# Optimization experiments

Measured on AMD Instinct MI355X. Metric: run time of the kernel, lower is better.

Reference implementation:

```python
import jax, jax.numpy as jnp
import numpy as np

N_QUBITS = 10
DEPTH = 3
KSIZE = 16
DILATION = 1
NFREQ = 8

I4 = np.eye(4, dtype=np.complex64)
XX4 = np.fliplr(np.eye(4)).astype(np.complex64)
YY4 = np.array([[0, 0, 0, -1], [0, 0, 1, 0], [0, 1, 0, 0], [-1, 0, 0, 0]], dtype=np.complex64)


def _u3(t, p, l):
    ct = jnp.cos(t / 2).astype(jnp.complex64)
    st = jnp.sin(t / 2).astype(jnp.complex64)
    ep, el = jnp.exp(1j * p), jnp.exp(1j * l)
    return jnp.stack([jnp.stack([ct, -el * st]), jnp.stack([ep * st, ep * el * ct])])


def _ising_zz(t):
    em, ep = jnp.exp(-0.5j * t), jnp.exp(0.5j * t)
    return jnp.diag(jnp.stack([em, ep, ep, em]))


def _ising_xx(t):
    return jnp.cos(t / 2) * I4 - 1j * jnp.sin(t / 2) * XX4


def _ising_yy(t):
    return jnp.cos(t / 2) * I4 - 1j * jnp.sin(t / 2) * YY4


def _cu3(t, p, l):
    # controlled-U3 (control = 1): deferred-measurement form of qml.cond(measure, U3)
    return jnp.eye(4, dtype=jnp.complex64).at[2:, 2:].set(_u3(t, p, l))


def _apply_1q(state, U, wire):
    s = jnp.moveaxis(state, 1 + wire, -1)
    if U.ndim == 3:  # per-sample gate (batched angles)
        s = jnp.einsum('bij,b...j->b...i', U, s)
    else:
        s = jnp.einsum('ij,...j->...i', U, s)
    return jnp.moveaxis(s, -1, 1 + wire)


def _apply_2q(state, U, w1, w2):
    s = jnp.moveaxis(state, (1 + w1, 1 + w2), (-2, -1))
    shp = s.shape
    s = s.reshape(shp[:-2] + (4,))
    s = jnp.einsum('ij,...j->...i', U, s)
    return jnp.moveaxis(s.reshape(shp), (-2, -1), (1 + w1, 1 + w2))


def _run_circuit(angles, freq_scale, conv_params, pool_params):
    Bm = angles.shape[0]
    state = jnp.zeros((Bm, 2 ** N_QUBITS), jnp.complex64).at[:, 0].set(1.0)
    state = state.reshape((Bm,) + (2,) * N_QUBITS)
    # frequency-matched encoding: RY(a) then RX(freq_scale * a), per-sample angles
    for i in range(N_QUBITS):
        a = angles[:, i]
        c = jnp.cos(a / 2).astype(jnp.complex64)
        s = jnp.sin(a / 2).astype(jnp.complex64)
        ry = jnp.stack([jnp.stack([c, -s], -1), jnp.stack([s, c], -1)], -2)
        state = _apply_1q(state, ry, i)
        b = freq_scale[i] * a
        cb = jnp.cos(b / 2).astype(jnp.complex64)
        sb = jnp.sin(b / 2).astype(jnp.complex64)
        rx = jnp.stack([jnp.stack([cb, -1j * sb], -1), jnp.stack([-1j * sb, cb], -1)], -2)
        state = _apply_1q(state, rx, i)
    wires = list(range(N_QUBITS))
    for layer in range(DEPTH):
        wp = conv_params[layer]
        nw = len(wires)
        for parity in (0, 1):
            for i2, w in enumerate(wires):
                if i2 % 2 == parity and i2 < nw - 1:
                    nxt = wires[i2 + 1]
                    state = _apply_1q(state, _u3(wp[i2, 0], wp[i2, 1], wp[i2, 2]), w)
                    state = _apply_1q(state, _u3(wp[i2 + 1, 3], wp[i2 + 1, 4], wp[i2 + 1, 5]), nxt)
                    state = _apply_2q(state, _ising_zz(wp[i2, 6]), w, nxt)
                    state = _apply_2q(state, _ising_yy(wp[i2, 7]), w, nxt)
                    state = _apply_2q(state, _ising_xx(wp[i2, 8]), w, nxt)
                    state = _apply_1q(state, _u3(wp[i2, 9], wp[i2, 10], wp[i2, 11]), w)
                    state = _apply_1q(state, _u3(wp[i2 + 1, 12], wp[i2 + 1, 13], wp[i2 + 1, 14]), nxt)
        pp = pool_params[layer]
        for i2, w in enumerate(wires):
            if i2 % 2 == 1:
                state = _apply_2q(state, _cu3(pp[i2 // 2, 0], pp[i2 // 2, 1], pp[i2 // 2, 2]), w, wires[i2 - 1])
        wires = wires[::2]
    p = jnp.abs(state) ** 2
    p = p.reshape(Bm, 2, -1).sum(-1)
    return p[:, 0] - p[:, 1]  # <Z_0>


def _forward(x, proj_w, proj_b, freq_scale, conv_params, pool_params, agg_weights):
    B, C, T = x.shape
    eff = DILATION * (KSIZE - 1)
    W = T - eff
    idx = jnp.arange(W)[:, None] + DILATION * jnp.arange(KSIZE)[None, :]  # [W,K]
    win = x[:, :, idx]  # [B,C,W,K]
    f = jnp.fft.rfft(win, axis=-1)[..., :NFREQ]  # [B,C,W,NF]
    feats = jnp.stack([jnp.log1p(jnp.abs(f)), jnp.angle(f) / jnp.pi], -1)  # [B,C,W,NF,2]
    feats = jnp.transpose(feats, (0, 2, 1, 3, 4)).reshape(B, W, -1)  # [B,W,C*NF*2]
    proj = jnp.tanh(feats @ proj_w.T + proj_b) * jnp.pi  # [B,W,n_qubits]
    ev = _run_circuit(proj.reshape(B * W, N_QUBITS), freq_scale, conv_params, pool_params)
    outs = ev.reshape(B, W)
    wts = jax.nn.softmax(agg_weights[:W])
    return (outs * wts[None, :]).sum(1)


def setup_inputs():
    key = jax.random.key(0)
    k = jax.random.split(key, 6)
    fft_dim = 22 * NFREQ * 2
    return {
        'x': jax.random.normal(k[0], (16, 22, 128), jnp.float32),
        'proj_w': jax.random.normal(k[1], (N_QUBITS, fft_dim), jnp.float32) / np.sqrt(fft_dim).astype(np.float32),
        'proj_b': jnp.zeros((N_QUBITS,), jnp.float32),
        'freq_scale': jnp.linspace(0.5, 3.0, N_QUBITS, dtype=jnp.float32),
        'conv_params': 0.1 * jax.random.normal(k[2], (DEPTH, N_QUBITS, 15), jnp.float32),
        'pool_params': 0.1 * jax.random.normal(k[3], (DEPTH, N_QUBITS // 2, 3), jnp.float32),
        'agg_weights': jnp.zeros((113,), jnp.float32),
    }


def reference(x, proj_w, proj_b, freq_scale, conv_params, pool_params, agg_weights):
    return _forward(x, proj_w, proj_b, freq_scale, conv_params, pool_params, agg_weights)
```

## Files before the change

### kernel.cpp

```cpp
#include <hip/hip_runtime.h>
#include <math.h>

#define NQ 10
#define WW 113
#define BB 16
#define CC 22
#define NF 8
#define FDIM 352
#define NS (BB*WW)
#define NGATE 23
#define SLOT(j) ((j) ^ (((j) >> 5) & 31))

#define WAVE_FENCE() do { \
    asm volatile("s_waitcnt lgkmcnt(0)" ::: "memory"); \
    __builtin_amdgcn_sched_barrier(0); \
} while (0)

__device__ __forceinline__ float2 cmul(float2 a, float2 b) {
    return make_float2(a.x*b.x - a.y*b.y, a.x*b.y + a.y*b.x);
}

__constant__ int G_KIND[NGATE]  = {0,0,0,0,0, 0,0,0,0, 1,1,1,1,1, 0,0,0,0, 1,1, 0,0, 1};
__constant__ int G_LAYER[NGATE] = {0,0,0,0,0, 0,0,0,0, 0,0,0,0,0, 1,1,1,1, 1,1, 2,2, 2};
__constant__ int G_IA[NGATE]    = {0,2,4,6,8, 1,3,5,7, 0,1,2,3,4, 0,2,1,3, 0,1, 0,1, 0};

__device__ void u3mat(float2* U, float th, float ph, float lm) {
    float ct, st, cp, sp, cl, sl;
    sincosf(th * 0.5f, &st, &ct);
    sincosf(ph, &sp, &cp);
    sincosf(lm, &sl, &cl);
    U[0] = make_float2(ct, 0.f);
    U[1] = make_float2(-cl * st, -sl * st);
    U[2] = make_float2(cp * st, sp * st);
    U[3] = make_float2((cp * cl - sp * sl) * ct, (sp * cl + cp * sl) * ct);
}

__device__ void mm4(float2* C, const float2* A, const float2* B) {
#pragma unroll
    for (int i = 0; i < 4; ++i)
#pragma unroll
        for (int j = 0; j < 4; ++j) {
            float2 acc = make_float2(0.f, 0.f);
#pragma unroll
            for (int k = 0; k < 4; ++k) {
                float2 p = cmul(A[i*4+k], B[k*4+j]);
                acc.x += p.x; acc.y += p.y;
            }
            C[i*4+j] = acc;
        }
}

__global__ __launch_bounds__(64) void prep_kernel(
    const float* __restrict__ conv,
    const float* __restrict__ pool,
    const float* __restrict__ aggw,
    float2* __restrict__ mats,
    float* __restrict__ wts,
    float* __restrict__ out)
{
    const int t = threadIdx.x;

    float a0 = (t < WW) ? aggw[t] : -1e30f;
    float a1 = (t + 64 < WW) ? aggw[t + 64] : -1e30f;
    float mx = fmaxf(a0, a1);
    for (int off = 32; off > 0; off >>= 1) mx = fmaxf(mx, __shfl_xor(mx, off));
    float e0 = (t < WW) ? expf(a0 - mx) : 0.f;
    float e1 = (t + 64 < WW) ? expf(a1 - mx) : 0.f;
    float es = e0 + e1;
    for (int off = 32; off > 0; off >>= 1) es += __shfl_xor(es, off);
    float inv = 1.0f / es;
    if (t < WW) wts[t] = e0 * inv;
    if (t + 64 < WW) wts[t + 64] = e1 * inv;
    if (t < BB) out[t] = 0.f;

    if (t >= NGATE) return;
    int kind = G_KIND[t], layer = G_LAYER[t], ia = G_IA[t];
    float2 F[16];
    if (kind == 0) {
        const float* wp = conv + layer * 150;
        float2 Uw0[4], Un0[4], Uw1[4], Un1[4];
        u3mat(Uw0, wp[ia*15+0], wp[ia*15+1], wp[ia*15+2]);
        u3mat(Un0, wp[(ia+1)*15+3], wp[(ia+1)*15+4], wp[(ia+1)*15+5]);
        u3mat(Uw1, wp[ia*15+9], wp[ia*15+10], wp[ia*15+11]);
        u3mat(Un1, wp[(ia+1)*15+12], wp[(ia+1)*15+13], wp[(ia+1)*15+14]);
        float2 Kpre[16], Kpost[16];
#pragma unroll
        for (int a = 0; a < 2; ++a)
#pragma unroll
        for (int b = 0; b < 2; ++b)
#pragma unroll
        for (int c = 0; c < 2; ++c)
#pragma unroll
        for (int d = 0; d < 2; ++d) {
            Kpre [(2*a+b)*4 + (2*c+d)] = cmul(Uw0[a*2+c], Un0[b*2+d]);
            Kpost[(2*a+b)*4 + (2*c+d)] = cmul(Uw1[a*2+c], Un1[b*2+d]);
        }
        float cz, sz, cy, sy, cx, sx;
        sincosf(wp[ia*15+6] * 0.5f, &sz, &cz);
        sincosf(wp[ia*15+7] * 0.5f, &sy, &cy);
        sincosf(wp[ia*15+8] * 0.5f, &sx, &cx);
        float2 Z[16], Y[16], X[16];
#pragma unroll
        for (int k = 0; k < 16; ++k) { Z[k] = make_float2(0,0); Y[k] = make_float2(0,0); X[k] = make_float2(0,0); }
        Z[0]  = make_float2(cz, -sz); Z[5]  = make_float2(cz, sz);
        Z[10] = make_float2(cz,  sz); Z[15] = make_float2(cz, -sz);
        Y[0] = Y[5] = Y[10] = Y[15] = make_float2(cy, 0);
        Y[0*4+3] = make_float2(0,  sy); Y[1*4+2] = make_float2(0, -sy);
        Y[2*4+1] = make_float2(0, -sy); Y[3*4+0] = make_float2(0,  sy);
        X[0] = X[5] = X[10] = X[15] = make_float2(cx, 0);
        X[0*4+3] = X[1*4+2] = X[2*4+1] = X[3*4+0] = make_float2(0, -sx);
        float2 T1[16], M[16], T2[16];
        mm4(T1, Y, Z);
        mm4(M, X, T1);
        mm4(T2, M, Kpre);
        mm4(F, Kpost, T2);
    } else {
        const float* pp = pool + layer * 15 + ia * 3;
        float2 U[4];
        u3mat(U, pp[0], pp[1], pp[2]);
#pragma unroll
        for (int k = 0; k < 16; ++k) F[k] = make_float2(0,0);
        F[0*4+0] = make_float2(1,0); F[1*4+1] = make_float2(1,0);
        F[2*4+2] = U[0]; F[2*4+3] = U[1];
        F[3*4+2] = U[2]; F[3*4+3] = U[3];
    }
#pragma unroll
    for (int k = 0; k < 16; ++k) mats[t*16 + k] = F[k];
}

template<int B3,int B2,int B1,int B0>
__device__ __forceinline__ int lanepart(int L) {
    constexpr int rm = (1<<B3)|(1<<B2)|(1<<B1)|(1<<B0);
    int idx = 0, lb = 5;
#pragma unroll
    for (int p = 9; p >= 0; --p)
        if (!((rm >> p) & 1)) { idx |= ((L >> lb) & 1) << p; --lb; }
    return idx;
}

template<int B3,int B2,int B1,int B0>
__device__ __forceinline__ int rpart(int r) {
    return (((r>>3)&1)<<B3) | (((r>>2)&1)<<B2) | (((r>>1)&1)<<B1) | ((r&1)<<B0);
}

template<int PA, int PB>
__device__ __forceinline__ void rgate(float2* amp, const float2* __restrict__ m)
{
    constexpr int mask = (1<<PA) | (1<<PB);
#pragma unroll
    for (int base = 0; base < 16; ++base) {
        if (base & mask) continue;
        float2 a0 = amp[base];
        float2 a1 = amp[base | (1<<PB)];
        float2 a2 = amp[base | (1<<PA)];
        float2 a3 = amp[base | mask];
        float2 nn[4];
#pragma unroll
        for (int g = 0; g < 4; ++g) {
            float2 m0 = m[g*4+0], m1 = m[g*4+1], m2 = m[g*4+2], m3 = m[g*4+3];
            float rx, ry;
            rx = m0.x*a0.x;            rx = fmaf(-m0.y, a0.y, rx);
            rx = fmaf(m1.x, a1.x, rx); rx = fmaf(-m1.y, a1.y, rx);
            rx = fmaf(m2.x, a2.x, rx); rx = fmaf(-m2.y, a2.y, rx);
            rx = fmaf(m3.x, a3.x, rx); rx = fmaf(-m3.y, a3.y, rx);
            ry = m0.x*a0.y;            ry = fmaf(m0.y, a0.x, ry);
            ry = fmaf(m1.x, a1.y, ry); ry = fmaf(m1.y, a1.x, ry);
            ry = fmaf(m2.x, a2.y, ry); ry = fmaf(m2.y, a2.x, ry);
            ry = fmaf(m3.x, a3.y, ry); ry = fmaf(m3.y, a3.x, ry);
            nn[g] = make_float2(rx, ry);
        }
        amp[base]           = nn[0];
        amp[base | (1<<PB)] = nn[1];
        amp[base | (1<<PA)] = nn[2];
        amp[base | mask]    = nn[3];
    }
}

template<int O3,int O2,int O1,int O0, int N3,int N2,int N1,int N0>
__device__ __forceinline__ void relayout(float2* wst, float2* amp, int L)
{
    const int lo = lanepart<O3,O2,O1,O0>(L);
#pragma unroll
    for (int r = 0; r < 16; ++r) {
        int idx = lo | rpart<O3,O2,O1,O0>(r);
        wst[SLOT(idx)] = amp[r];
    }
    WAVE_FENCE();
    const int ln = lanepart<N3,N2,N1,N0>(L);
#pragma unroll
    for (int r = 0; r < 16; ++r) {
        int idx = ln | rpart<N3,N2,N1,N0>(r);
        amp[r] = wst[SLOT(idx)];
    }
    WAVE_FENCE();
}

__global__ __launch_bounds__(256) void fused_kernel(
    const float* __restrict__ x,
    const float* __restrict__ proj_w,
    const float* __restrict__ proj_b,
    const float* __restrict__ freq_scale,
    const float2* __restrict__ mats,
    const float* __restrict__ wts,
    float* __restrict__ out)
{
    const int tid  = threadIdx.x;
    const int wave = tid >> 6;
    const int L    = tid & 63;
    const int s = blockIdx.x * 4 + wave;
    const int b = s / WW, w = s % WW;

    __shared__ float2 wst_all[4][1024];
    float2* wst = wst_all[wave];

    float*  win  = (float*)wst;
    float*  feat = (float*)wst + 384;
    float2* tw   = wst + 400;
    float2* vq   = wst + 416;
    float*  angs = (float*)wst + 880;

    const float* xb = x + b * (CC * 128) + w;
    for (int e = L; e < CC * 16; e += 64) {
        int c = e >> 4, n = e & 15;
        win[e] = xb[c * 128 + n];
    }
    if (L < 16) {
        float ang = -(float)M_PI * (float)L * 0.125f;
        float sv, cv; sincosf(ang, &sv, &cv);
        tw[L] = make_float2(cv, sv);
    }
    WAVE_FENCE();

    for (int pidx = L; pidx < CC * NF; pidx += 64) {
        int c = pidx >> 3, k = pidx & 7;
        float re = 0.f, im = 0.f;
#pragma unroll
        for (int n = 0; n < 16; ++n) {
            int m = (k * n) & 15;
            float2 t = tw[m];
            float xv = win[c * 16 + n];
            re = fmaf(xv, t.x, re);
            im = fmaf(xv, t.y, im);
        }
        feat[c * 16 + (k << 1)]     = log1pf(sqrtf(re * re + im * im));
        feat[c * 16 + (k << 1) + 1] = atan2f(im, re) * (float)(1.0 / M_PI);
    }
    WAVE_FENCE();

    {
        float fv[6];
#pragma unroll
        for (int k = 0; k < 6; ++k) {
            int e = L + 64 * k;
            fv[k] = (e < FDIM) ? feat[e] : 0.f;
        }
        for (int q = 0; q < NQ; ++q) {
            const float* pw = proj_w + q * FDIM + L;
            float acc = 0.f;
#pragma unroll
            for (int k = 0; k < 6; ++k) {
                float wv = (L + 64 * k < FDIM) ? pw[64 * k] : 0.f;
                acc = fmaf(fv[k], wv, acc);
            }
#pragma unroll
            for (int off = 32; off > 0; off >>= 1) acc += __shfl_xor(acc, off);
            if (L == 0) angs[q] = acc;
        }
    }
    WAVE_FENCE();

    if (L < NQ) {
        float a = tanhf(angs[L] + proj_b[L]) * (float)M_PI;
        float bf = freq_scale[L] * a;
        float ca, sa, cb, sb;
        sincosf(a * 0.5f, &sa, &ca);
        sincosf(bf * 0.5f, &sb, &cb);
        vq[2 * L]     = make_float2(cb * ca, -sb * sa);
        vq[2 * L + 1] = make_float2(cb * sa, -sb * ca);
    }
    WAVE_FENCE();

    float2 amp[16];
    {
        float2 pre = make_float2(1.f, 0.f);
#pragma unroll
        for (int p = 0; p < 6; ++p) {
            float2 f = vq[2 * (9 - p) + ((L >> p) & 1)];
            pre = cmul(pre, f);
        }
        float2 p98[4], p76[4];
#pragma unroll
        for (int i = 0; i < 4; ++i) {
            p98[i] = cmul(vq[2 * 0 + (i >> 1)], vq[2 * 1 + (i & 1)]);
            p76[i] = cmul(vq[2 * 2 + (i >> 1)], vq[2 * 3 + (i & 1)]);
        }
#pragma unroll
        for (int r = 0; r < 16; ++r)
            amp[r] = cmul(pre, cmul(p98[r >> 2], p76[r & 3]));
    }
    WAVE_FENCE();

    rgate<3,2>(amp, mats + 0*16);
    rgate<1,0>(amp, mats + 1*16);
    rgate<2,1>(amp, mats + 5*16);
    rgate<2,3>(amp, mats + 9*16);
    relayout<9,8,7,6, 5,4,3,2>(wst, amp, L);
    rgate<3,2>(amp, mats + 2*16);
    rgate<1,0>(amp, mats + 3*16);
    rgate<2,1>(amp, mats + 7*16);
    relayout<5,4,3,2, 7,6,5,4>(wst, amp, L);
    rgate<2,1>(amp, mats + 6*16);
    rgate<2,3>(amp, mats + 10*16);
    rgate<0,1>(amp, mats + 11*16);
    relayout<7,6,5,4, 3,2,1,0>(wst, amp, L);
    rgate<1,0>(amp, mats + 4*16);
    rgate<2,1>(amp, mats + 8*16);
    rgate<2,3>(amp, mats + 12*16);
    rgate<0,1>(amp, mats + 13*16);
    relayout<3,2,1,0, 9,7,5,3>(wst, amp, L);
    rgate<3,2>(amp, mats + 14*16);
    rgate<1,0>(amp, mats + 15*16);
    rgate<2,1>(amp, mats + 16*16);
    rgate<2,3>(amp, mats + 18*16);
    relayout<9,7,5,3, 9,5,3,1>(wst, amp, L);
    rgate<1,0>(amp, mats + 17*16);
    rgate<1,2>(amp, mats + 19*16);
    rgate<3,2>(amp, mats + 20*16);
    rgate<2,0>(amp, mats + 21*16);
    rgate<2,3>(amp, mats + 22*16);

    float local = 0.f;
#pragma unroll
    for (int r = 0; r < 16; ++r) {
        float p = amp[r].x * amp[r].x + amp[r].y * amp[r].y;
        local += (r & 8) ? -p : p;
    }
#pragma unroll
    for (int off = 32; off > 0; off >>= 1) local += __shfl_xor(local, off);
    if (L == 0) atomicAdd(&out[b], local * wts[w]);
}

extern "C" void kernel_launch(void* const* d_in, const int* in_sizes, int n_in,
                              void* d_out, int out_size, void* d_ws, size_t ws_size,
                              hipStream_t stream)
{
    const float* x           = (const float*)d_in[0];
    const float* proj_w      = (const float*)d_in[1];
    const float* proj_b      = (const float*)d_in[2];
    const float* freq_scale  = (const float*)d_in[3];
    const float* conv_params = (const float*)d_in[4];
    const float* pool_params = (const float*)d_in[5];
    const float* aggw        = (const float*)d_in[6];
    float* out = (float*)d_out;

    float2* mats = (float2*)d_ws;
    float* wts   = (float*)d_ws + NGATE * 16 * 2;

    prep_kernel<<<1, 64, 0, stream>>>(conv_params, pool_params, aggw, mats, wts, out);
    fused_kernel<<<NS / 4, 256, 0, stream>>>(x, proj_w, proj_b, freq_scale, mats, wts, out);
}
```

Baseline: 126.2 us.

## Parallelize gate-matrix prep per element, specialize pool gates, use single-wave blocks

```diff
diff --git a/kernel.cpp b/kernel.cpp
--- a/kernel.cpp
+++ b/kernel.cpp
@@ -9,22 +9,22 @@
 #define FDIM 352
 #define NS (BB*WW)
 #define NGATE 23
-#define SLOT(j) ((j) ^ (((j) >> 5) & 31))
-
-#define WAVE_FENCE() do { \
-    asm volatile("s_waitcnt lgkmcnt(0)" ::: "memory"); \
-    __builtin_amdgcn_sched_barrier(0); \
-} while (0)
-
-__device__ __forceinline__ float2 cmul(float2 a, float2 b) {
+
+__device__ __forceinline__ constexpr int SLOT(int j) { return j ^ ((j >> 5) & 31); }
+
+__device__ __forceinline__ float2 cmulf(float2 a, float2 b) {
     return make_float2(a.x*b.x - a.y*b.y, a.x*b.y + a.y*b.x);
+}
+__device__ __forceinline__ void cmacf(float2& acc, float2 c, float2 v) {
+    acc.x = fmaf(c.x, v.x, acc.x); acc.x = fmaf(-c.y, v.y, acc.x);
+    acc.y = fmaf(c.x, v.y, acc.y); acc.y = fmaf(c.y, v.x, acc.y);
 }
 
 __constant__ int G_KIND[NGATE]  = {0,0,0,0,0, 0,0,0,0, 1,1,1,1,1, 0,0,0,0, 1,1, 0,0, 1};
 __constant__ int G_LAYER[NGATE] = {0,0,0,0,0, 0,0,0,0, 0,0,0,0,0, 1,1,1,1, 1,1, 2,2, 2};
 __constant__ int G_IA[NGATE]    = {0,2,4,6,8, 1,3,5,7, 0,1,2,3,4, 0,2,1,3, 0,1, 0,1, 0};
 
-__device__ void u3mat(float2* U, float th, float ph, float lm) {
+__device__ __forceinline__ void u3mat(float2* U, float th, float ph, float lm) {
     float ct, st, cp, sp, cl, sl;
     sincosf(th * 0.5f, &st, &ct);
     sincosf(ph, &sp, &cp);
@@ -35,22 +35,7 @@
     U[3] = make_float2((cp * cl - sp * sl) * ct, (sp * cl + cp * sl) * ct);
 }
 
-__device__ void mm4(float2* C, const float2* A, const float2* B) {
-#pragma unroll
-    for (int i = 0; i < 4; ++i)
-#pragma unroll
-        for (int j = 0; j < 4; ++j) {
-            float2 acc = make_float2(0.f, 0.f);
-#pragma unroll
-            for (int k = 0; k < 4; ++k) {
-                float2 p = cmul(A[i*4+k], B[k*4+j]);
-                acc.x += p.x; acc.y += p.y;
-            }
-            C[i*4+j] = acc;
-        }
-}
-
-__global__ __launch_bounds__(64) void prep_kernel(
+__global__ __launch_bounds__(384) void prep_kernel(
     const float* __restrict__ conv,
     const float* __restrict__ pool,
     const float* __restrict__ aggw,
@@ -60,73 +45,68 @@
 {
     const int t = threadIdx.x;
 
-    float a0 = (t < WW) ? aggw[t] : -1e30f;
-    float a1 = (t + 64 < WW) ? aggw[t + 64] : -1e30f;
-    float mx = fmaxf(a0, a1);
-    for (int off = 32; off > 0; off >>= 1) mx = fmaxf(mx, __shfl_xor(mx, off));
-    float e0 = (t < WW) ? expf(a0 - mx) : 0.f;
-    float e1 = (t + 64 < WW) ? expf(a1 - mx) : 0.f;
-    float es = e0 + e1;
-    for (int off = 32; off > 0; off >>= 1) es += __shfl_xor(es, off);
-    float inv = 1.0f / es;
-    if (t < WW) wts[t] = e0 * inv;
-    if (t + 64 < WW) wts[t + 64] = e1 * inv;
-    if (t < BB) out[t] = 0.f;
-
-    if (t >= NGATE) return;
-    int kind = G_KIND[t], layer = G_LAYER[t], ia = G_IA[t];
-    float2 F[16];
-    if (kind == 0) {
+    if (t < 64) {
+        float a0 = (t < WW) ? aggw[t] : -1e30f;
+        float a1 = (t + 64 < WW) ? aggw[t + 64] : -1e30f;
+        float mx = fmaxf(a0, a1);
+        for (int off = 32; off > 0; off >>= 1) mx = fmaxf(mx, __shfl_xor(mx, off));
+        float e0 = (t < WW) ? expf(a0 - mx) : 0.f;
+        float e1 = (t + 64 < WW) ? expf(a1 - mx) : 0.f;
+        float es = e0 + e1;
+        for (int off = 32; off > 0; off >>= 1) es += __shfl_xor(es, off);
+        float inv = 1.0f / es;
+        if (t < WW) wts[t] = e0 * inv;
+        if (t + 64 < WW) wts[t + 64] = e1 * inv;
+        if (t < BB) out[t] = 0.f;
+    }
+
+    if (t >= NGATE * 16) return;
+    const int g = t >> 4, k = t & 15;
+    const int i = k >> 2, j = k & 3;
+    const int kind = G_KIND[g], layer = G_LAYER[g], ia = G_IA[g];
+    float2 F;
+    if (kind == 1) {
+        const float* pp = pool + layer * 15 + ia * 3;
+        if (i < 2 || j < 2) {
+            F = (i == j) ? make_float2(1.f, 0.f) : make_float2(0.f, 0.f);
+        } else {
+            float2 U[4];
+            u3mat(U, pp[0], pp[1], pp[2]);
+            F = U[(i - 2) * 2 + (j - 2)];
+        }
+    } else {
         const float* wp = conv + layer * 150;
         float2 Uw0[4], Un0[4], Uw1[4], Un1[4];
-        u3mat(Uw0, wp[ia*15+0], wp[ia*15+1], wp[ia*15+2]);
-        u3mat(Un0, wp[(ia+1)*15+3], wp[(ia+1)*15+4], wp[(ia+1)*15+5]);
-        u3mat(Uw1, wp[ia*15+9], wp[ia*15+10], wp[ia*15+11]);
+        u3mat(Uw0, wp[ia*15+0],  wp[ia*15+1],  wp[ia*15+2]);
+        u3mat(Un0, wp[(ia+1)*15+3],  wp[(ia+1)*15+4],  wp[(ia+1)*15+5]);
+        u3mat(Uw1, wp[ia*15+9],  wp[ia*15+10], wp[ia*15+11]);
         u3mat(Un1, wp[(ia+1)*15+12], wp[(ia+1)*15+13], wp[(ia+1)*15+14]);
-        float2 Kpre[16], Kpost[16];
-#pragma unroll
-        for (int a = 0; a < 2; ++a)
-#pragma unroll
-        for (int b = 0; b < 2; ++b)
-#pragma unroll
-        for (int c = 0; c < 2; ++c)
-#pragma unroll
-        for (int d = 0; d < 2; ++d) {
-            Kpre [(2*a+b)*4 + (2*c+d)] = cmul(Uw0[a*2+c], Un0[b*2+d]);
-            Kpost[(2*a+b)*4 + (2*c+d)] = cmul(Uw1[a*2+c], Un1[b*2+d]);
-        }
         float cz, sz, cy, sy, cx, sx;
         sincosf(wp[ia*15+6] * 0.5f, &sz, &cz);
         sincosf(wp[ia*15+7] * 0.5f, &sy, &cy);
         sincosf(wp[ia*15+8] * 0.5f, &sx, &cx);
-        float2 Z[16], Y[16], X[16];
-#pragma unroll
-        for (int k = 0; k < 16; ++k) { Z[k] = make_float2(0,0); Y[k] = make_float2(0,0); X[k] = make_float2(0,0); }
-        Z[0]  = make_float2(cz, -sz); Z[5]  = make_float2(cz, sz);
-        Z[10] = make_float2(cz,  sz); Z[15] = make_float2(cz, -sz);
-        Y[0] = Y[5] = Y[10] = Y[15] = make_float2(cy, 0);
-        Y[0*4+3] = make_float2(0,  sy); Y[1*4+2] = make_float2(0, -sy);
-        Y[2*4+1] = make_float2(0, -sy); Y[3*4+0] = make_float2(0,  sy);
-        X[0] = X[5] = X[10] = X[15] = make_float2(cx, 0);
-        X[0*4+3] = X[1*4+2] = X[2*4+1] = X[3*4+0] = make_float2(0, -sx);
-        float2 T1[16], M[16], T2[16];
-        mm4(T1, Y, Z);
-        mm4(M, X, T1);
-        mm4(T2, M, Kpre);
-        mm4(F, Kpost, T2);
-    } else {
-        const float* pp = pool + layer * 15 + ia * 3;
-        float2 U[4];
-        u3mat(U, pp[0], pp[1], pp[2]);
-#pragma unroll
-        for (int k = 0; k < 16; ++k) F[k] = make_float2(0,0);
-        F[0*4+0] = make_float2(1,0); F[1*4+1] = make_float2(1,0);
-        F[2*4+2] = U[0]; F[2*4+3] = U[1];
-        F[3*4+2] = U[2]; F[3*4+3] = U[3];
-    }
-#pragma unroll
-    for (int k = 0; k < 16; ++k) mats[t*16 + k] = F[k];
-}
+        float2 acc = make_float2(0.f, 0.f);
+#pragma unroll
+        for (int a = 0; a < 4; ++a) {
+            const float sa = (a == 0 || a == 3) ? 1.f : -1.f;
+            const float2 za = (a == 0 || a == 3) ? make_float2(cz, -sz)
+                                                 : make_float2(cz,  sz);
+            const float daa = fmaf(sa * sx, sy, cx * cy);
+            const float oaa = fmaf(sa * sy, cx, -sx * cy);
+            float2 Mdiag = make_float2(daa * za.x, daa * za.y);
+            float2 Moff  = make_float2(-oaa * za.y, oaa * za.x);
+            float2 kpost = cmulf(Uw1[(i >> 1) * 2 + (a >> 1)], Un1[(i & 1) * 2 + (a & 1)]);
+            float2 kpreA = cmulf(Uw0[(a >> 1) * 2 + (j >> 1)], Un0[(a & 1) * 2 + (j & 1)]);
+            float2 kpreN = cmulf(Uw0[(1 - (a >> 1)) * 2 + (j >> 1)], Un0[(1 - (a & 1)) * 2 + (j & 1)]);
+            float2 inner = cmulf(Mdiag, kpreA);
+            cmacf(inner, Moff, kpreN);
+            cmacf(acc, kpost, inner);
+        }
+        F = acc;
+    }
+    mats[g * 16 + k] = F;
+}
+
 
 template<int B3,int B2,int B1,int B0>
 __device__ __forceinline__ int lanepart(int L) {
@@ -154,25 +134,32 @@
         float2 a1 = amp[base | (1<<PB)];
         float2 a2 = amp[base | (1<<PA)];
         float2 a3 = amp[base | mask];
-        float2 nn[4];
+        float2 n[4];
 #pragma unroll
         for (int g = 0; g < 4; ++g) {
-            float2 m0 = m[g*4+0], m1 = m[g*4+1], m2 = m[g*4+2], m3 = m[g*4+3];
-            float rx, ry;
-            rx = m0.x*a0.x;            rx = fmaf(-m0.y, a0.y, rx);
-            rx = fmaf(m1.x, a1.x, rx); rx = fmaf(-m1.y, a1.y, rx);
-            rx = fmaf(m2.x, a2.x, rx); rx = fmaf(-m2.y, a2.y, rx);
-            rx = fmaf(m3.x, a3.x, rx); rx = fmaf(-m3.y, a3.y, rx);
-            ry = m0.x*a0.y;            ry = fmaf(m0.y, a0.x, ry);
-            ry = fmaf(m1.x, a1.y, ry); ry = fmaf(m1.y, a1.x, ry);
-            ry = fmaf(m2.x, a2.y, ry); ry = fmaf(m2.y, a2.x, ry);
-            ry = fmaf(m3.x, a3.y, ry); ry = fmaf(m3.y, a3.x, ry);
-            nn[g] = make_float2(rx, ry);
-        }
-        amp[base]           = nn[0];
-        amp[base | (1<<PB)] = nn[1];
-        amp[base | (1<<PA)] = nn[2];
-        amp[base | mask]    = nn[3];
+            float2 acc = cmulf(m[g*4+0], a0);
+            cmacf(acc, m[g*4+1], a1);
+            cmacf(acc, m[g*4+2], a2);
+            cmacf(acc, m[g*4+3], a3);
+            n[g] = acc;
+        }
+        amp[base]           = n[0];
+        amp[base | (1<<PB)] = n[1];
+        amp[base | (1<<PA)] = n[2];
+        amp[base | mask]    = n[3];
+    }
+}
+
+template<int CR, int TR>
+__device__ __forceinline__ void rr_pool(float2* amp, const float2* __restrict__ m)
+{
+#pragma unroll
+    for (int r = 0; r < 16; ++r) {
+        if (!((r >> CR) & 1) || ((r >> TR) & 1)) continue;
+        float2 a2 = amp[r], a3 = amp[r | (1<<TR)];
+        float2 n2 = cmulf(m[10], a2); cmacf(n2, m[11], a3);
+        float2 n3 = cmulf(m[14], a2); cmacf(n3, m[15], a3);
+        amp[r] = n2; amp[r | (1<<TR)] = n3;
     }
 }
 
@@ -182,20 +169,18 @@
     const int lo = lanepart<O3,O2,O1,O0>(L);
 #pragma unroll
     for (int r = 0; r < 16; ++r) {
-        int idx = lo | rpart<O3,O2,O1,O0>(r);
+        const int idx = lo | rpart<O3,O2,O1,O0>(r);
         wst[SLOT(idx)] = amp[r];
     }
-    WAVE_FENCE();
     const int ln = lanepart<N3,N2,N1,N0>(L);
 #pragma unroll
     for (int r = 0; r < 16; ++r) {
-        int idx = ln | rpart<N3,N2,N1,N0>(r);
+        const int idx = ln | rpart<N3,N2,N1,N0>(r);
         amp[r] = wst[SLOT(idx)];
     }
-    WAVE_FENCE();
-}
-
-__global__ __launch_bounds__(256) void fused_kernel(
+}
+
+__global__ __launch_bounds__(64) void fused_kernel(
     const float* __restrict__ x,
     const float* __restrict__ proj_w,
     const float* __restrict__ proj_b,
@@ -204,15 +189,11 @@
     const float* __restrict__ wts,
     float* __restrict__ out)
 {
-    const int tid  = threadIdx.x;
-    const int wave = tid >> 6;
-    const int L    = tid & 63;
-    const int s = blockIdx.x * 4 + wave;
+    const int s = blockIdx.x;
     const int b = s / WW, w = s % WW;
-
-    __shared__ float2 wst_all[4][1024];
-    float2* wst = wst_all[wave];
-
+    const int L = threadIdx.x;
+
+    __shared__ float2 wst[1024];
     float*  win  = (float*)wst;
     float*  feat = (float*)wst + 384;
     float2* tw   = wst + 400;
@@ -220,24 +201,27 @@
     float*  angs = (float*)wst + 880;
 
     const float* xb = x + b * (CC * 128) + w;
-    for (int e = L; e < CC * 16; e += 64) {
-        int c = e >> 4, n = e & 15;
-        win[e] = xb[c * 128 + n];
+#pragma unroll
+    for (int kk = 0; kk < 6; ++kk) {
+        int e = L + 64 * kk;
+        if (e < CC * 16) {
+            int c = e >> 4, n = e & 15;
+            win[e] = xb[c * 128 + n];
+        }
     }
     if (L < 16) {
         float ang = -(float)M_PI * (float)L * 0.125f;
         float sv, cv; sincosf(ang, &sv, &cv);
         tw[L] = make_float2(cv, sv);
     }
-    WAVE_FENCE();
 
     for (int pidx = L; pidx < CC * NF; pidx += 64) {
         int c = pidx >> 3, k = pidx & 7;
         float re = 0.f, im = 0.f;
 #pragma unroll
         for (int n = 0; n < 16; ++n) {
-            int m = (k * n) & 15;
-            float2 t = tw[m];
+            int mm = (k * n) & 15;
+            float2 t = tw[mm];
             float xv = win[c * 16 + n];
             re = fmaf(xv, t.x, re);
             im = fmaf(xv, t.y, im);
@@ -245,7 +229,6 @@
         feat[c * 16 + (k << 1)]     = log1pf(sqrtf(re * re + im * im));
         feat[c * 16 + (k << 1) + 1] = atan2f(im, re) * (float)(1.0 / M_PI);
     }
-    WAVE_FENCE();
 
     {
         float fv[6];
@@ -267,7 +250,6 @@
             if (L == 0) angs[q] = acc;
         }
     }
-    WAVE_FENCE();
 
     if (L < NQ) {
         float a = tanhf(angs[L] + proj_b[L]) * (float)M_PI;
@@ -278,7 +260,6 @@
         vq[2 * L]     = make_float2(cb * ca, -sb * sa);
         vq[2 * L + 1] = make_float2(cb * sa, -sb * ca);
     }
-    WAVE_FENCE();
 
     float2 amp[16];
     {
@@ -286,48 +267,47 @@
 #pragma unroll
         for (int p = 0; p < 6; ++p) {
             float2 f = vq[2 * (9 - p) + ((L >> p) & 1)];
-            pre = cmul(pre, f);
+            pre = cmulf(pre, f);
         }
         float2 p98[4], p76[4];
 #pragma unroll
         for (int i = 0; i < 4; ++i) {
-            p98[i] = cmul(vq[2 * 0 + (i >> 1)], vq[2 * 1 + (i & 1)]);
-            p76[i] = cmul(vq[2 * 2 + (i >> 1)], vq[2 * 3 + (i & 1)]);
+            p98[i] = cmulf(vq[2 * 0 + (i >> 1)], vq[2 * 1 + (i & 1)]);
+            p76[i] = cmulf(vq[2 * 2 + (i >> 1)], vq[2 * 3 + (i & 1)]);
         }
 #pragma unroll
         for (int r = 0; r < 16; ++r)
-            amp[r] = cmul(pre, cmul(p98[r >> 2], p76[r & 3]));
-    }
-    WAVE_FENCE();
+            amp[r] = cmulf(pre, cmulf(p98[r >> 2], p76[r & 3]));
+    }
 
     rgate<3,2>(amp, mats + 0*16);
     rgate<1,0>(amp, mats + 1*16);
     rgate<2,1>(amp, mats + 5*16);
-    rgate<2,3>(amp, mats + 9*16);
+    rr_pool<2,3>(amp, mats + 9*16);
     relayout<9,8,7,6, 5,4,3,2>(wst, amp, L);
     rgate<3,2>(amp, mats + 2*16);
     rgate<1,0>(amp, mats + 3*16);
     rgate<2,1>(amp, mats + 7*16);
     relayout<5,4,3,2, 7,6,5,4>(wst, amp, L);
     rgate<2,1>(amp, mats + 6*16);
-    rgate<2,3>(amp, mats + 10*16);
-    rgate<0,1>(amp, mats + 11*16);
+    rr_pool<2,3>(amp, mats + 10*16);
+    rr_pool<0,1>(amp, mats + 11*16);
     relayout<7,6,5,4, 3,2,1,0>(wst, amp, L);
     rgate<1,0>(amp, mats + 4*16);
     rgate<2,1>(amp, mats + 8*16);
-    rgate<2,3>(amp, mats + 12*16);
-    rgate<0,1>(amp, mats + 13*16);
+    rr_pool<2,3>(amp, mats + 12*16);
+    rr_pool<0,1>(amp, mats + 13*16);
     relayout<3,2,1,0, 9,7,5,3>(wst, amp, L);
     rgate<3,2>(amp, mats + 14*16);
     rgate<1,0>(amp, mats + 15*16);
     rgate<2,1>(amp, mats + 16*16);
-    rgate<2,3>(amp, mats + 18*16);
+    rr_pool<2,3>(amp, mats + 18*16);
     relayout<9,7,5,3, 9,5,3,1>(wst, amp, L);
     rgate<1,0>(amp, mats + 17*16);
-    rgate<1,2>(amp, mats + 19*16);
+    rr_pool<1,2>(amp, mats + 19*16);
     rgate<3,2>(amp, mats + 20*16);
     rgate<2,0>(amp, mats + 21*16);
-    rgate<2,3>(amp, mats + 22*16);
+    rr_pool<2,3>(amp, mats + 22*16);
 
     float local = 0.f;
 #pragma unroll
@@ -356,6 +336,6 @@
     float2* mats = (float2*)d_ws;
     float* wts   = (float*)d_ws + NGATE * 16 * 2;
 
-    prep_kernel<<<1, 64, 0, stream>>>(conv_params, pool_params, aggw, mats, wts, out);
-    fused_kernel<<<NS / 4, 256, 0, stream>>>(x, proj_w, proj_b, freq_scale, mats, wts, out);
-}
+    prep_kernel<<<1, 384, 0, stream>>>(conv_params, pool_params, aggw, mats, wts, out);
+    fused_kernel<<<NS, 64, 0, stream>>>(x, proj_w, proj_b, freq_scale, mats, wts, out);
+}
```

Result: faster. 116.2 us (-8.0%).
